# Kernel optimization log

Measured on AMD Instinct MI355X. Metric: run time of the kernel, lower is better.

Reference implementation:

```python
import jax, jax.numpy as jnp
import numpy as np

B, N, F, NCG, NCONV, VOCAB = 16, 1024, 128, 64, 3, 100
EPS = 0.001


def setup_inputs() -> dict:
    key = jax.random.key(0)
    ks = jax.random.split(key, 16)
    atoms_nodes = jax.random.randint(ks[0], (B, N), 0, VOCAB, dtype=jnp.int32)
    xyz = jax.random.normal(ks[1], (B, N, 3), jnp.float32) * 3.0
    # chain bonds (i, i+1) per molecule -> every atom has degree >= 1
    bi = jnp.repeat(jnp.arange(B), N - 1)
    si = jnp.tile(jnp.arange(N - 1), B)
    bonds = jnp.stack([bi, si, si + 1], axis=1).astype(jnp.int32)  # [B*(N-1), 3]
    tau = jnp.float32(1.0)
    gumbel_u = jax.random.uniform(ks[2], (B, N, NCG), jnp.float32, 1e-6, 1.0 - 1e-6)
    # parameters
    emb = jax.random.normal(ks[3], (VOCAB, F), jnp.float32) * 0.1
    emb = emb.at[0].set(0.0)  # padding_idx=0
    s = 1.0 / np.sqrt(F)
    upd_W1 = jax.random.uniform(ks[4], (NCONV, F, F), jnp.float32, -s, s)
    upd_b1 = jax.random.uniform(ks[5], (NCONV, F), jnp.float32, -s, s)
    upd_W2 = jax.random.uniform(ks[6], (NCONV, F, F), jnp.float32, -s, s)
    upd_b2 = jax.random.uniform(ks[7], (NCONV, F), jnp.float32, -s, s)
    cg_W1 = jax.random.uniform(ks[8], (F, F), jnp.float32, -s, s)
    cg_b1 = jax.random.uniform(ks[9], (F,), jnp.float32, -s, s)
    cg_W2 = jax.random.uniform(ks[10], (F, NCG), jnp.float32, -s, s)
    cg_b2 = jax.random.uniform(ks[11], (NCG,), jnp.float32, -s, s)
    return {"atoms_nodes": atoms_nodes, "xyz": xyz, "bonds": bonds, "tau": tau,
            "gumbel_u": gumbel_u, "emb": emb,
            "upd_W1": upd_W1, "upd_b1": upd_b1, "upd_W2": upd_W2, "upd_b2": upd_b2,
            "cg_W1": cg_W1, "cg_b1": cg_b1, "cg_W2": cg_W2, "cg_b2": cg_b2}


def reference(atoms_nodes, xyz, bonds, tau, gumbel_u, emb,
              upd_W1, upd_b1, upd_W2, upd_b2, cg_W1, cg_b1, cg_W2, cg_b2):
    h = emb[atoms_nodes]  # [B,N,F]
    # dense symmetric adjacency from bond list
    adj = jnp.zeros((B, N, N), jnp.float32)
    adj = adj.at[bonds[:, 0], bonds[:, 1], bonds[:, 2]].set(1.0)
    adj = adj.at[bonds[:, 0], bonds[:, 2], bonds[:, 1]].set(1.0)
    deg = jnp.sum(adj, axis=-1)[:, :, None]  # [B,N,1]
    for l in range(NCONV):
        ch = jnp.tanh(h @ upd_W1[l] + upd_b1[l]) @ upd_W2[l] + upd_b2[l]
        dh = jnp.einsum('bif,bij->bjf', ch, adj) / deg
        h = h + dh
    # gumbel-softmax assignment (soft)
    assign_logits = jnp.tanh(h @ cg_W1 + cg_b1) @ cg_W2 + cg_b2  # [B,N,NCG]
    g = -jnp.log(-jnp.log(gumbel_u))
    M = jax.nn.softmax((assign_logits + g) / tau, axis=-1)  # [B,N,NCG]
    M_norm = M / jnp.sum(M, axis=-2, keepdims=True)
    H = jnp.einsum('bnj,bnf->bjf', M_norm, h)        # [B,NCG,F]
    cg_xyz = jnp.einsum('bin,bij->bjn', xyz, M_norm)  # [B,NCG,3]
    cg_adj = jnp.broadcast_to(jnp.ones((NCG, NCG)) - jnp.eye(NCG), (B, NCG, NCG))
    diff = cg_xyz[:, :, None, :] - cg_xyz[:, None, :, :]
    dist = jnp.sqrt(jnp.sum(diff * diff, axis=-1) + EPS)  # [B,NCG,NCG]
    knbrs = jnp.argsort(dist, axis=-1)
    return (M, M_norm, h, H, adj, cg_xyz, cg_adj, knbrs)
```

## Files before the change

### kernel.cpp

```cpp
#include <hip/hip_runtime.h>
#include <math.h>

#define BB 16
#define NN 1024
#define FF 128
#define NCG 64
#define NCONV 3
#define CAP 8

typedef double f64x4 __attribute__((ext_vector_type(4)));

static const size_t O_M     = 0;
static const size_t O_MN    = (size_t)BB*NN*NCG;
static const size_t O_H     = O_MN  + (size_t)BB*NN*NCG;
static const size_t O_HH    = O_H   + (size_t)BB*NN*FF;
static const size_t O_ADJ   = O_HH  + (size_t)BB*NCG*FF;
static const size_t O_CGXYZ = O_ADJ + (size_t)BB*NN*NN;
static const size_t O_CGADJ = O_CGXYZ + (size_t)BB*NCG*3;
static const size_t O_KN    = O_CGADJ + (size_t)BB*NCG*NCG;

static const size_t S_H64   = 0;
static const size_t S_T64   = 2097152;
static const size_t S_C64   = 4194304;
static const size_t S_LM64  = 0;
static const size_t S_HPF   = 6291456;
static const size_t S_CGP   = 7340032;
static const size_t S_W64   = 7503872;

static const size_t WO_CGW1 = 98304;
static const size_t WO_CGW2 = 114688;
static const int    W64_N   = 122880;

static const size_t W_COLS = 0;
static const size_t W_CNT  = (size_t)BB*NCG;
static const size_t W_NBR  = W_CNT + (size_t)BB*NN/2;

__global__ void k_init(const int* __restrict__ atoms, const float* __restrict__ emb,
                       const float* __restrict__ uW1, const float* __restrict__ uW2,
                       const float* __restrict__ cgW1, const float* __restrict__ cgW2,
                       double* __restrict__ W64, float* __restrict__ cgadj,
                       int* __restrict__ cnt, double* __restrict__ colsum,
                       double* __restrict__ h64) {
    int i = blockIdx.x * blockDim.x + threadIdx.x;
    if (i < BB*NN) cnt[i] = 0;
    if (i < BB*NCG) colsum[i] = 0.0;
    if (i < W64_N) {
        float v;
        if (i < 98304) {
            int l = i >> 15, r = i & 32767;
            v = (r < 16384) ? uW1[l*16384 + r] : uW2[l*16384 + (r & 16383)];
        } else if (i < 114688) v = cgW1[i - 98304];
        else                   v = cgW2[i - 114688];
        W64[i] = (double)v;
    }
    if (i < BB*NCG*NCG) {
        int r = (i / NCG) % NCG, cjj = i % NCG;
        cgadj[i] = (r == cjj) ? 0.f : 1.f;
    }
    if (i < BB*NN*(FF/4)) {
        int n = i / (FF/4), f4 = i % (FF/4);
        int a = atoms[n];
        const float4 v = *reinterpret_cast<const float4*>(&emb[(size_t)a*FF + f4*4]);
        double* hp = &h64[(size_t)n*FF + f4*4];
        hp[0] = (double)v.x; hp[1] = (double)v.y; hp[2] = (double)v.z; hp[3] = (double)v.w;
    }
}

__global__ void k_build_nbr(const int* __restrict__ bonds, int nb, int* cnt, int* nbr) {
    int i = blockIdx.x * blockDim.x + threadIdx.x;
    if (i >= nb) return;
    int b = bonds[i*3+0], s = bonds[i*3+1], t = bonds[i*3+2];
    int ns = b*NN + s, nt = b*NN + t;
    int p = atomicAdd(&cnt[ns], 1);
    if (p < CAP) nbr[(size_t)ns*CAP + p] = nt;
    int q = atomicAdd(&cnt[nt], 1);
    if (q < CAP) nbr[(size_t)nt*CAP + q] = ns;
}

template<int COUTT, bool TANH>
__global__ __launch_bounds__(256) void k_gemm_mfma(const double* __restrict__ in,
                                                   const double* __restrict__ W,
                                                   const float* __restrict__ bias,
                                                   double* __restrict__ out) {
    constexpr int K = 128, KC = 32;
    constexpr int CT2 = COUTT/2;
    __shared__ double As[64*34];
    __shared__ double Ws[KC*66];
    const int tid = threadIdx.x;
    const int col0 = blockIdx.y * 64;
    const int C02 = col0 >> 1;
    const size_t row0 = (size_t)blockIdx.x * 64;
    const double2* in2 = reinterpret_cast<const double2*>(in + row0*K);
    const double2* Wg2 = reinterpret_cast<const double2*>(W);
    double2* As2 = reinterpret_cast<double2*>(As);
    double2* Ws2 = reinterpret_cast<double2*>(Ws);

    double2 pA[4], pW[4];
    #pragma unroll
    for (int i = 0; i < 4; ++i) { int q = tid + i*256; pA[i] = in2[(q>>4)*64 + (q&15)]; }
    #pragma unroll
    for (int i = 0; i < 4; ++i) { int q = tid + i*256; pW[i] = Wg2[(q>>5)*CT2 + C02 + (q&31)]; }

    const int lane = tid & 63;
    const int wv = tid >> 6;
    const int m = lane & 15, kq = lane >> 4;
    const int arow = (wv*16 + m)*34 + kq;

    f64x4 acc[4];
    #pragma unroll
    for (int ct = 0; ct < 4; ++ct) acc[ct] = (f64x4){0.0, 0.0, 0.0, 0.0};

    for (int kc = 0; kc < K; kc += KC) {
        __syncthreads();
        #pragma unroll
        for (int i = 0; i < 4; ++i) { int q = tid + i*256; As2[(q>>4)*17 + (q&15)] = pA[i]; }
        #pragma unroll
        for (int i = 0; i < 4; ++i) { int q = tid + i*256; Ws2[(q>>5)*33 + (q&31)] = pW[i]; }
        if (kc + KC < K) {
            const int kn = kc + KC, kn2 = kn >> 1;
            #pragma unroll
            for (int i = 0; i < 4; ++i) { int q = tid + i*256; pA[i] = in2[(q>>4)*64 + kn2 + (q&15)]; }
            #pragma unroll
            for (int i = 0; i < 4; ++i) { int q = tid + i*256; pW[i] = Wg2[(kn + (q>>5))*CT2 + C02 + (q&31)]; }
        }
        __syncthreads();
        #pragma unroll
        for (int kk = 0; kk < KC; kk += 4) {
            double a = As[arow + kk];
            const double* wrow = Ws + (kk + kq)*66 + m;
            #pragma unroll
            for (int ct = 0; ct < 4; ++ct) {
                double b = wrow[ct*16];
                acc[ct] = __builtin_amdgcn_mfma_f64_16x16x4f64(a, b, acc[ct], 0, 0, 0);
            }
        }
    }

    const int orow = wv*16 + kq*4;
    #pragma unroll
    for (int ct = 0; ct < 4; ++ct) {
        int c = col0 + ct*16 + m;
        double bv = (double)bias[c];
        #pragma unroll
        for (int i = 0; i < 4; ++i) {
            double v = acc[ct][i] + bv;
            if (TANH) v = tanh(v);
            out[(row0 + orow + i)*COUTT + c] = v;
        }
    }
}

template<bool WRITE_F32>
__global__ void k_gather(const double* __restrict__ ch, const int* __restrict__ nbr,
                         const int* __restrict__ cnt, double* __restrict__ h,
                         float* __restrict__ hout) {
    int idx = blockIdx.x * blockDim.x + threadIdx.x;
    if (idx >= BB*NN*(FF/4)) return;
    int node = idx >> 5, f4 = idx & 31;
    int c = cnt[node];
    double2 s0; s0.x = 0.0; s0.y = 0.0;
    double2 s1 = s0;
    for (int q = 0; q < c; ++q) {
        int nb = nbr[(size_t)node*CAP + q];
        const double2* cp = reinterpret_cast<const double2*>(ch + (size_t)nb*FF + f4*4);
        double2 a = cp[0], b2 = cp[1];
        s0.x += a.x; s0.y += a.y; s1.x += b2.x; s1.y += b2.y;
    }
    double w = c > 0 ? 1.0/(double)c : 0.0;
    double2* hp = reinterpret_cast<double2*>(h + (size_t)node*FF + f4*4);
    double2 h0 = hp[0], h1 = hp[1];
    h0.x += s0.x*w; h0.y += s0.y*w; h1.x += s1.x*w; h1.y += s1.y*w;
    hp[0] = h0; hp[1] = h1;
    if (WRITE_F32) {
        float4 o; o.x = (float)h0.x; o.y = (float)h0.y; o.z = (float)h1.x; o.w = (float)h1.y;
        *reinterpret_cast<float4*>(&hout[(size_t)node*FF + f4*4]) = o;
    }
}

__global__ __launch_bounds__(256) void k_softmax64(double* __restrict__ lm,
                            const float* __restrict__ gum,
                            const float* __restrict__ tau_p, float* __restrict__ M_out,
                            double* __restrict__ colsum) {
    __shared__ double red[256];
    int row = blockIdx.x * 4 + threadIdx.x / 64;
    int lane = threadIdx.x & 63;
    double tau = (double)(*tau_p);
    double u = (double)gum[(size_t)row*NCG + lane];
    double g = -log(-log(u));
    double v = (lm[(size_t)row*NCG + lane] + g) / tau;
    double m = v;
    #pragma unroll
    for (int off = 32; off; off >>= 1) m = fmax(m, __shfl_xor(m, off));
    double e = exp(v - m);
    double s = e;
    #pragma unroll
    for (int off = 32; off; off >>= 1) s += __shfl_xor(s, off);
    double mv = e / s;
    lm[(size_t)row*NCG + lane] = mv;
    M_out[(size_t)row*NCG + lane] = (float)mv;
    red[threadIdx.x] = mv;
    __syncthreads();
    if (threadIdx.x < 64) {
        int b = row >> 10;
        atomicAdd(&colsum[b*NCG + lane],
                  red[lane] + red[64+lane] + red[128+lane] + red[192+lane]);
    }
}

__global__ void k_mnorm_out(const double* __restrict__ M, const double* __restrict__ colsum,
                            float* __restrict__ Mn) {
    size_t i = (size_t)blockIdx.x * blockDim.x + threadIdx.x;
    if (i >= (size_t)BB*NN*NCG) return;
    size_t b = i >> 16;
    int j = (int)(i & 63);
    Mn[i] = (float)(M[i] / colsum[b*NCG + j]);
}

__global__ __launch_bounds__(256) void k_Hpart32(const float* __restrict__ Mn,
                                                 const float* __restrict__ h,
                                                 float* __restrict__ Hp) {
    __shared__ float Ms[32*NCG];
    __shared__ float hs[32*FF];
    const int b = blockIdx.x, ch = blockIdx.y;
    const int tid = threadIdx.x;
    const int tc = tid % 32, tr = tid / 32;
    const float4* M4 = reinterpret_cast<const float4*>(Mn + (size_t)b*NN*NCG);
    const float4* h4 = reinterpret_cast<const float4*>(h + (size_t)b*NN*FF);
    float4* Ms4 = reinterpret_cast<float4*>(Ms);
    float4* hs4 = reinterpret_cast<float4*>(hs);
    const float2* Ms2 = reinterpret_cast<const float2*>(Ms);
    const float2* hs2 = reinterpret_cast<const float2*>(hs);

    float acc[8][4];
    #pragma unroll
    for (int i = 0; i < 8; ++i)
        #pragma unroll
        for (int j = 0; j < 4; ++j) acc[i][j] = 0.f;

    for (int s = 0; s < 2; ++s) {
        const int n0 = ch*64 + s*32;
        __syncthreads();
        #pragma unroll
        for (int i = 0; i < 2; ++i) Ms4[tid + i*256] = M4[n0*16 + tid + i*256];
        #pragma unroll
        for (int i = 0; i < 4; ++i) hs4[tid + i*256] = h4[n0*32 + tid + i*256];
        __syncthreads();
        for (int n = 0; n < 32; ++n) {
            float2 hv0 = hs2[n*64 + tc];
            float2 hv1 = hs2[n*64 + 32 + tc];
            float2 m0 = Ms2[n*32 + tr];
            float2 m1 = Ms2[n*32 + 8 + tr];
            float2 m2 = Ms2[n*32 + 16 + tr];
            float2 m3 = Ms2[n*32 + 24 + tr];
            float mj[8] = {m0.x, m0.y, m1.x, m1.y, m2.x, m2.y, m3.x, m3.y};
            #pragma unroll
            for (int jj = 0; jj < 8; ++jj) {
                acc[jj][0] += mj[jj]*hv0.x; acc[jj][1] += mj[jj]*hv0.y;
                acc[jj][2] += mj[jj]*hv1.x; acc[jj][3] += mj[jj]*hv1.y;
            }
        }
    }
    float* Ho = Hp + ((size_t)ch*BB + b) * NCG * FF;
    #pragma unroll
    for (int gj = 0; gj < 4; ++gj)
        #pragma unroll
        for (int pj = 0; pj < 2; ++pj) {
            int j = tr*2 + gj*16 + pj;
            int jj = gj*2 + pj;
            float2 o0; o0.x = acc[jj][0]; o0.y = acc[jj][1];
            float2 o1; o1.x = acc[jj][2]; o1.y = acc[jj][3];
            float2* op = reinterpret_cast<float2*>(Ho + (size_t)j*FF);
            op[tc] = o0; op[32 + tc] = o1;
        }
}

__global__ void k_Hfin32(const float* __restrict__ Hp, float* __restrict__ H) {
    int idx = blockIdx.x * blockDim.x + threadIdx.x;
    if (idx >= BB*NCG*FF) return;
    int b = idx / (NCG*FF);
    int r = idx % (NCG*FF);
    float s = 0.f;
    #pragma unroll
    for (int c = 0; c < 16; ++c) s += Hp[((size_t)c*BB + b)*NCG*FF + r];
    H[idx] = s;
}

__global__ __launch_bounds__(192) void k_cgpart(const double* __restrict__ M,
                                                const float* __restrict__ xyz,
                                                double* __restrict__ cgp) {
    __shared__ double Ms[32*NCG];
    __shared__ double xs[32*3];
    const int b = blockIdx.x, ch = blockIdx.y;
    const int tid = threadIdx.x;
    const int j = tid / 3, d = tid % 3;
    const int n0 = ch*32;
    const double2* M2 = reinterpret_cast<const double2*>(M + (size_t)b*NN*NCG);
    double2* Ms2 = reinterpret_cast<double2*>(Ms);
    const float* xb = xyz + (size_t)b*NN*3;
    for (int q = tid; q < 1024; q += 192) Ms2[q] = M2[n0*32 + q];
    for (int q = tid; q < 96; q += 192) xs[q] = (double)xb[n0*3 + q];
    __syncthreads();
    double acc = 0.0;
    #pragma unroll 8
    for (int n = 0; n < 32; ++n) acc += Ms[n*NCG + j] * xs[n*3 + d];
    cgp[((size_t)ch*BB + b)*192 + tid] = acc;
}

__global__ __launch_bounds__(1024) void k_knbrs(const double* __restrict__ cgp,
                                                const double* __restrict__ colsum,
                                                float* __restrict__ o_cg,
                                                float* __restrict__ kn) {
    __shared__ double cs[NCG*3];
    const int b = blockIdx.x;
    const int tid = threadIdx.x;
    if (tid < NCG*3) {
        double s = 0.0;
        #pragma unroll
        for (int c = 0; c < 32; ++c) s += cgp[((size_t)c*BB + b)*192 + tid];
        double v = s / colsum[b*NCG + tid/3];
        cs[tid] = v;
        if (blockIdx.y == 0) o_cg[(size_t)b*192 + tid] = (float)v;
    }
    __syncthreads();
    const int i = blockIdx.y * 16 + tid / 64;
    const int j = tid & 63;
    double xi = cs[i*3+0], yi = cs[i*3+1], zi = cs[i*3+2];
    double dxj = xi - cs[j*3+0], dyj = yi - cs[j*3+1], dzj = zi - cs[j*3+2];
    double d2j = dxj*dxj + dyj*dyj + dzj*dzj;
    int rank = 0;
    for (int k = 0; k < NCG; ++k) {
        double dx = xi - cs[k*3+0], dy = yi - cs[k*3+1], dz = zi - cs[k*3+2];
        double d2k = dx*dx + dy*dy + dz*dz;
        rank += (d2k < d2j) || (d2k == d2j && k < j);
    }
    kn[(size_t)b*NCG*NCG + (size_t)i*NCG + rank] = (float)j;
}

__global__ __launch_bounds__(256) void k_adj(const int* __restrict__ cnt,
                                             const int* __restrict__ nbr,
                                             float4* __restrict__ adj4) {
    const int node = blockIdx.x;
    const int t = threadIdx.x;
    const int col0 = t*4;
    int c = cnt[node];
    if (c > CAP) c = CAP;
    float4 v; v.x = v.y = v.z = v.w = 0.f;
    for (int q = 0; q < c; ++q) {
        int dst = nbr[(size_t)node*CAP + q] & (NN-1);
        int d = dst - col0;
        if (d == 0) v.x = 1.f;
        else if (d == 1) v.y = 1.f;
        else if (d == 2) v.z = 1.f;
        else if (d == 3) v.w = 1.f;
    }
    adj4[(size_t)node*256 + t] = v;
}

extern "C" void kernel_launch(void* const* d_in, const int* in_sizes, int n_in,
                              void* d_out, int out_size, void* d_ws, size_t ws_size,
                              hipStream_t stream) {
    const int*   atoms  = (const int*)  d_in[0];
    const float* xyz    = (const float*)d_in[1];
    const int*   bonds  = (const int*)  d_in[2];
    const float* tau    = (const float*)d_in[3];
    const float* gum    = (const float*)d_in[4];
    const float* emb    = (const float*)d_in[5];
    const float* uW1    = (const float*)d_in[6];
    const float* ub1    = (const float*)d_in[7];
    const float* uW2    = (const float*)d_in[8];
    const float* ub2    = (const float*)d_in[9];
    const float* cgW1   = (const float*)d_in[10];
    const float* cgb1   = (const float*)d_in[11];
    const float* cgW2   = (const float*)d_in[12];
    const float* cgb2   = (const float*)d_in[13];

    float* out = (float*)d_out;
    float* o_M   = out + O_M;
    float* o_Mn  = out + O_MN;
    float* o_h   = out + O_H;
    float* o_H   = out + O_HH;
    float* o_adj = out + O_ADJ;
    float* o_cg  = out + O_CGXYZ;
    float* o_ca  = out + O_CGADJ;
    float* o_kn  = out + O_KN;

    double* scr   = (double*)o_adj;
    double* h64   = scr + S_H64;
    double* t64   = scr + S_T64;
    double* c64   = scr + S_C64;
    double* lm64  = scr + S_LM64;
    float*  Hpf   = (float*)(scr + S_HPF);
    double* cgp   = scr + S_CGP;
    double* W64   = scr + S_W64;

    double* wsd    = (double*)d_ws;
    double* colsum = wsd + W_COLS;
    int*    cnt    = (int*)(wsd + W_CNT);
    int*    nbr    = (int*)(wsd + W_NBR);

    const int nb = in_sizes[2] / 3;

    hipLaunchKernelGGL(k_init, dim3(2048), dim3(256), 0, stream,
                       atoms, emb, uW1, uW2, cgW1, cgW2, W64, o_ca, cnt, colsum, h64);
    hipLaunchKernelGGL(k_build_nbr, dim3((nb+255)/256), dim3(256), 0, stream,
                       bonds, nb, cnt, nbr);

    for (int l = 0; l < NCONV; ++l) {
        hipLaunchKernelGGL((k_gemm_mfma<128,true>), dim3(256,2), dim3(256), 0, stream,
                           h64, W64 + (size_t)l*32768, ub1 + (size_t)l*FF, t64);
        hipLaunchKernelGGL((k_gemm_mfma<128,false>), dim3(256,2), dim3(256), 0, stream,
                           t64, W64 + (size_t)l*32768 + 16384, ub2 + (size_t)l*FF, c64);
        if (l < NCONV-1)
            hipLaunchKernelGGL((k_gather<false>), dim3(2048), dim3(256), 0, stream,
                               c64, nbr, cnt, h64, o_h);
        else
            hipLaunchKernelGGL((k_gather<true>), dim3(2048), dim3(256), 0, stream,
                               c64, nbr, cnt, h64, o_h);
    }

    hipLaunchKernelGGL((k_gemm_mfma<128,true>), dim3(256,2), dim3(256), 0, stream,
                       h64, W64 + WO_CGW1, cgb1, t64);
    hipLaunchKernelGGL((k_gemm_mfma<64,false>), dim3(256,1), dim3(256), 0, stream,
                       t64, W64 + WO_CGW2, cgb2, lm64);

    hipLaunchKernelGGL(k_softmax64, dim3(4096), dim3(256), 0, stream,
                       lm64, gum, tau, o_M, colsum);
    hipLaunchKernelGGL(k_mnorm_out, dim3(4096), dim3(256), 0, stream, lm64, colsum, o_Mn);
    hipLaunchKernelGGL(k_Hpart32, dim3(BB, 16), dim3(256), 0, stream, o_Mn, o_h, Hpf);
    hipLaunchKernelGGL(k_Hfin32, dim3(512), dim3(256), 0, stream, Hpf, o_H);
    hipLaunchKernelGGL(k_cgpart, dim3(BB, 32), dim3(192), 0, stream, lm64, xyz, cgp);
    hipLaunchKernelGGL(k_knbrs, dim3(BB, 4), dim3(1024), 0, stream,
                       cgp, colsum, o_cg, o_kn);

    hipLaunchKernelGGL(k_adj, dim3(BB*NN), dim3(256), 0, stream,
                       cnt, nbr, (float4*)o_adj);
}
```

Measured before the change: 361.2 us.

## Fuse M normalization into H partial kernel and widen GEMM K-chunk to 64

The standalone M_norm kernel is removed. k_Hpart32 now reads the double-precision softmax output and column sums, divides in-kernel, writes M_norm to global and uses the values directly from shared memory. This avoids one launch plus a separate read/write pass over M_norm. Separately, the fp64 MFMA GEMM K chunk grows from 32 to 64, halving the sync iterations at the cost of more LDS and more prefetch registers, which may lower occupancy.

Result: slower. 369.2 us (+2.2%).

```diff
diff --git a/kernel.cpp b/kernel.cpp
--- a/kernel.cpp
+++ b/kernel.cpp
@@ -82,9 +82,9 @@
                                                    const double* __restrict__ W,
                                                    const float* __restrict__ bias,
                                                    double* __restrict__ out) {
-    constexpr int K = 128, KC = 32;
+    constexpr int K = 128, KC = 64;
     constexpr int CT2 = COUTT/2;
-    __shared__ double As[64*34];
+    __shared__ double As[64*66];
     __shared__ double Ws[KC*66];
     const int tid = threadIdx.x;
     const int col0 = blockIdx.y * 64;
@@ -95,16 +95,16 @@
     double2* As2 = reinterpret_cast<double2*>(As);
     double2* Ws2 = reinterpret_cast<double2*>(Ws);
 
-    double2 pA[4], pW[4];
-    #pragma unroll
-    for (int i = 0; i < 4; ++i) { int q = tid + i*256; pA[i] = in2[(q>>4)*64 + (q&15)]; }
-    #pragma unroll
-    for (int i = 0; i < 4; ++i) { int q = tid + i*256; pW[i] = Wg2[(q>>5)*CT2 + C02 + (q&31)]; }
+    double2 pA[8], pW[8];
+    #pragma unroll
+    for (int i = 0; i < 8; ++i) { int q = tid + i*256; pA[i] = in2[(q>>5)*64 + (q&31)]; }
+    #pragma unroll
+    for (int i = 0; i < 8; ++i) { int q = tid + i*256; pW[i] = Wg2[(q>>5)*CT2 + C02 + (q&31)]; }
 
     const int lane = tid & 63;
     const int wv = tid >> 6;
     const int m = lane & 15, kq = lane >> 4;
-    const int arow = (wv*16 + m)*34 + kq;
+    const int arow = (wv*16 + m)*66 + kq;
 
     f64x4 acc[4];
     #pragma unroll
@@ -113,15 +113,15 @@
     for (int kc = 0; kc < K; kc += KC) {
         __syncthreads();
         #pragma unroll
-        for (int i = 0; i < 4; ++i) { int q = tid + i*256; As2[(q>>4)*17 + (q&15)] = pA[i]; }
-        #pragma unroll
-        for (int i = 0; i < 4; ++i) { int q = tid + i*256; Ws2[(q>>5)*33 + (q&31)] = pW[i]; }
+        for (int i = 0; i < 8; ++i) { int q = tid + i*256; As2[(q>>5)*33 + (q&31)] = pA[i]; }
+        #pragma unroll
+        for (int i = 0; i < 8; ++i) { int q = tid + i*256; Ws2[(q>>5)*33 + (q&31)] = pW[i]; }
         if (kc + KC < K) {
             const int kn = kc + KC, kn2 = kn >> 1;
             #pragma unroll
-            for (int i = 0; i < 4; ++i) { int q = tid + i*256; pA[i] = in2[(q>>4)*64 + kn2 + (q&15)]; }
+            for (int i = 0; i < 8; ++i) { int q = tid + i*256; pA[i] = in2[(q>>5)*64 + kn2 + (q&31)]; }
             #pragma unroll
-            for (int i = 0; i < 4; ++i) { int q = tid + i*256; pW[i] = Wg2[(kn + (q>>5))*CT2 + C02 + (q&31)]; }
+            for (int i = 0; i < 8; ++i) { int q = tid + i*256; pW[i] = Wg2[(kn + (q>>5))*CT2 + C02 + (q&31)]; }
         }
         __syncthreads();
         #pragma unroll
@@ -207,30 +207,27 @@
     }
 }
 
-__global__ void k_mnorm_out(const double* __restrict__ M, const double* __restrict__ colsum,
-                            float* __restrict__ Mn) {
-    size_t i = (size_t)blockIdx.x * blockDim.x + threadIdx.x;
-    if (i >= (size_t)BB*NN*NCG) return;
-    size_t b = i >> 16;
-    int j = (int)(i & 63);
-    Mn[i] = (float)(M[i] / colsum[b*NCG + j]);
-}
-
-__global__ __launch_bounds__(256) void k_Hpart32(const float* __restrict__ Mn,
+__global__ __launch_bounds__(256) void k_Hpart32(const double* __restrict__ M,
+                                                 const double* __restrict__ colsum,
                                                  const float* __restrict__ h,
+                                                 float* __restrict__ Mn,
                                                  float* __restrict__ Hp) {
     __shared__ float Ms[32*NCG];
     __shared__ float hs[32*FF];
+    __shared__ double cs64[NCG];
     const int b = blockIdx.x, ch = blockIdx.y;
     const int tid = threadIdx.x;
     const int tc = tid % 32, tr = tid / 32;
-    const float4* M4 = reinterpret_cast<const float4*>(Mn + (size_t)b*NN*NCG);
+    const double2* M2 = reinterpret_cast<const double2*>(M + (size_t)b*NN*NCG);
     const float4* h4 = reinterpret_cast<const float4*>(h + (size_t)b*NN*FF);
-    float4* Ms4 = reinterpret_cast<float4*>(Ms);
+    float2* Mn2g = reinterpret_cast<float2*>(Mn + (size_t)b*NN*NCG);
+    float2* Ms2w = reinterpret_cast<float2*>(Ms);
     float4* hs4 = reinterpret_cast<float4*>(hs);
     const float2* Ms2 = reinterpret_cast<const float2*>(Ms);
     const float2* hs2 = reinterpret_cast<const float2*>(hs);
 
+    if (tid < NCG) cs64[tid] = colsum[b*NCG + tid];
+
     float acc[8][4];
     #pragma unroll
     for (int i = 0; i < 8; ++i)
@@ -241,7 +238,16 @@
         const int n0 = ch*64 + s*32;
         __syncthreads();
         #pragma unroll
-        for (int i = 0; i < 2; ++i) Ms4[tid + i*256] = M4[n0*16 + tid + i*256];
+        for (int i = 0; i < 4; ++i) {
+            int q = tid + i*256;
+            int jj2 = q & 31;
+            double2 mv = M2[n0*32 + q];
+            float2 o;
+            o.x = (float)(mv.x / cs64[jj2*2]);
+            o.y = (float)(mv.y / cs64[jj2*2+1]);
+            Ms2w[q] = o;
+            Mn2g[n0*32 + q] = o;
+        }
         #pragma unroll
         for (int i = 0; i < 4; ++i) hs4[tid + i*256] = h4[n0*32 + tid + i*256];
         __syncthreads();
@@ -425,8 +431,8 @@
 
     hipLaunchKernelGGL(k_softmax64, dim3(4096), dim3(256), 0, stream,
                        lm64, gum, tau, o_M, colsum);
-    hipLaunchKernelGGL(k_mnorm_out, dim3(4096), dim3(256), 0, stream, lm64, colsum, o_Mn);
-    hipLaunchKernelGGL(k_Hpart32, dim3(BB, 16), dim3(256), 0, stream, o_Mn, o_h, Hpf);
+    hipLaunchKernelGGL(k_Hpart32, dim3(BB, 16), dim3(256), 0, stream,
+                       lm64, colsum, o_h, o_Mn, Hpf);
     hipLaunchKernelGGL(k_Hfin32, dim3(512), dim3(256), 0, stream, Hpf, o_H);
     hipLaunchKernelGGL(k_cgpart, dim3(BB, 32), dim3(192), 0, stream, lm64, xyz, cgp);
     hipLaunchKernelGGL(k_knbrs, dim3(BB, 4), dim3(1024), 0, stream,
```
